# Kernel tuning notes

Measured on AMD Instinct MI355X. Metric: run time of the kernel, lower is better.

## Reference

```python
import jax, jax.numpy as jnp
import numpy as np
from jax import lax

B = 128
NC = 100


def _conv(x, w, b, stride=1, pad=0, groups=1):
    y = lax.conv_general_dilated(x, w, (stride, stride), [(pad, pad), (pad, pad)],
                                 dimension_numbers=('NCHW', 'OIHW', 'NCHW'),
                                 feature_group_count=groups)
    return y + b[None, :, None, None]


def _maxpool(x):
    # kernel 3, stride 2 (ceil_mode is a no-op for 55/27/13 inputs)
    return lax.reduce_window(x, -jnp.inf, lax.max, (1, 1, 3, 3), (1, 1, 2, 2), 'VALID')


def _lrn(x, n=5, alpha=1e-4, beta=0.75, k=1.0):
    # torch.nn.LocalResponseNorm: x / (k + alpha/n * sum_window(x^2))**beta
    s = lax.reduce_window(x * x, 0.0, lax.add, (1, n, 1, 1), (1, 1, 1, 1),
                          [(0, 0), (n // 2, n // 2), (0, 0), (0, 0)])
    return x / (k + (alpha / n) * s) ** beta


def _features(x, w1, b1, w2, b2, w3, b3, w4, b4, w5, b5):
    x = _lrn(_maxpool(jnp.maximum(_conv(x, w1, b1, 4, 0), 0)))
    x = _lrn(_maxpool(jnp.maximum(_conv(x, w2, b2, 1, 2, 2), 0)))
    x = jnp.maximum(_conv(x, w3, b3, 1, 1), 0)
    x = jnp.maximum(_conv(x, w4, b4, 1, 1, 2), 0)
    x = _maxpool(jnp.maximum(_conv(x, w5, b5, 1, 1, 2), 0))
    return x  # [B,256,6,6]


def _head(f, w6, b6, w7, b7, wc, bc):
    h = jnp.maximum(f @ w6.T + b6, 0)
    h = jnp.maximum(h @ w7.T + b7, 0)
    return h @ wc.T + bc


def setup_inputs():
    key = jax.random.key(0)
    ks = jax.random.split(key, 12)
    p = lambda k, s, sc: jax.random.normal(k, s, jnp.float32) * sc
    return {
        'x': jax.random.normal(ks[0], (B, 3, 227, 227), jnp.float32),
        'gt': jax.random.randint(ks[1], (B,), 0, NC),
        'u': jax.random.uniform(ks[2], (B, 36), jnp.float32),
        'flag': 1,
        'w1': p(ks[3], (96, 3, 11, 11), 0.02), 'b1': jnp.zeros((96,), jnp.float32),
        'w2': p(ks[4], (256, 48, 5, 5), 0.02), 'b2': jnp.zeros((256,), jnp.float32),
        'w3': p(ks[5], (384, 256, 3, 3), 0.02), 'b3': jnp.zeros((384,), jnp.float32),
        'w4': p(ks[6], (384, 192, 3, 3), 0.02), 'b4': jnp.zeros((384,), jnp.float32),
        'w5': p(ks[7], (256, 192, 3, 3), 0.02), 'b5': jnp.zeros((256,), jnp.float32),
        'w6': p(ks[8], (4096, 9216), 0.01), 'b6': jnp.zeros((4096,), jnp.float32),
        'w7': p(ks[9], (4096, 4096), 0.01), 'b7': jnp.zeros((4096,), jnp.float32),
        'wc': p(ks[10], (NC, 4096), 0.01), 'bc': jnp.zeros((NC,), jnp.float32),
    }


def reference(x, gt, u, flag, w1, b1, w2, b2, w3, b3, w4, b4, w5, b5,
              w6, b6, w7, b7, wc, bc):
    feat = _features(x * 57.6, w1, b1, w2, b2, w3, b3, w4, b4, w5, b5)
    Bn, C, H, W = feat.shape
    HW = H * W
    head = lambda f: _head(f.reshape(Bn, -1), w6, b6, w7, b7, wc, bc)
    if flag:
        rows = jnp.arange(Bn)
        xn = lax.stop_gradient(feat)  # detached clone in torch
        def score(f):
            out = head(f)
            return jnp.sum(out[rows, gt]), out
        grads, out = jax.grad(score, has_aux=True)(xn)
        # ---- spatial RSC branch (deterministic stand-in for random.randint<=4) ----
        spatial_mean = grads.mean(axis=1).reshape(Bn, HW)
        drop_num = HW // 3  # int(HW/3)
        th = -jnp.sort(-spatial_mean, axis=1)[:, drop_num:drop_num + 1]
        cand = spatial_mean >= th               # high-gradient cells (mask_all==0 in torch)
        sc = jnp.where(cand, u, -1.0)           # npr.choice(zero_index, drop_num) equivalent
        _, idx = lax.top_k(sc, drop_num)
        mask = jnp.ones((Bn, HW), feat.dtype).at[rows[:, None], idx].set(0.0)
        mask_all = mask.reshape(Bn, 1, H, W)
        # ---- keep masks only where dropping them hurts the gt probability ----
        cls_before = jax.nn.softmax(out, axis=1)[rows, gt]
        cls_after = jax.nn.softmax(head(xn * mask_all), axis=1)[rows, gt]
        cv = jnp.maximum(cls_before - cls_after - 1e-4, 0.0)
        th_fg = -jnp.sort(-cv)[int(round(Bn / 3.0))]
        keep_full = ~(cv > th_fg)
        mask_all = jnp.where(keep_full[:, None, None, None], jnp.float32(1.0), mask_all)
        feat = feat * lax.stop_gradient(mask_all)
    return head(feat)
```

## Files before the change

kernel.cpp:

```cpp
#include <hip/hip_runtime.h>

#define CDIV(a,b) (((a)+(b)-1)/(b))

typedef __attribute__((ext_vector_type(8))) short bf16x8;
typedef __attribute__((ext_vector_type(4))) float f32x4;

__device__ __forceinline__ unsigned packsplit(float x) {
    union { float f; unsigned u; } a; a.f = x;
    unsigned r = a.u + 0x7fffu + ((a.u >> 16) & 1u);
    unsigned hi = r & 0xffff0000u;
    union { float f; unsigned u; } b; b.u = hi;
    float res = x - b.f;
    union { float f; unsigned u; } c; c.f = res;
    unsigned r2 = c.u + 0x7fffu + ((c.u >> 16) & 1u);
    return hi | (r2 >> 16);
}
__device__ __forceinline__ unsigned hipair(unsigned a, unsigned b){ return (a>>16)|(b&0xffff0000u); }
__device__ __forceinline__ unsigned lopair(unsigned a, unsigned b){ return (a&0xffffu)|(b<<16); }

__global__ void pack_scale_kernel(const float* __restrict__ src, unsigned* __restrict__ dst,
                                  int n4, float scale)
{
    int i = blockIdx.x * blockDim.x + threadIdx.x;
    if (i >= n4) return;
    float4 v = ((const float4*)src)[i];
    uint4 o;
    o.x = packsplit(v.x * scale); o.y = packsplit(v.y * scale);
    o.z = packsplit(v.z * scale); o.w = packsplit(v.w * scale);
    ((uint4*)dst)[i] = o;
}

__global__ void wsplit_frag(const float* __restrict__ w, short* __restrict__ dst,
                            int G, int cog, int R, int CB, int niter)
{
    int idx = blockIdx.x * blockDim.x + threadIdx.x;
    int total = G * CB * niter * 512;
    if (idx >= total) return;
    int ln = idx & 63;
    int t  = (idx >> 6) & 7;
    int s  = idx >> 9;
    int kt = s % niter;
    int s2 = s / niter;
    int cb = s2 % CB;
    int g  = s2 / CB;
    int row = cb * 128 + t * 16 + (ln & 15);
    int qq = ln >> 4;
    bool rok = row < cog;
    const float* wr = w + (size_t)(g * cog + (rok ? row : 0)) * R;
    short hv[8], lv[8];
    #pragma unroll
    for (int e = 0; e < 8; ++e) {
        int k = kt * 32 + ((e < 4) ? (qq * 4 + e) : (16 + qq * 4 + e - 4));
        float x = (rok && k < R) ? wr[k] : 0.f;
        unsigned p = packsplit(x);
        hv[e] = (short)(p >> 16);
        lv[e] = (short)(p & 0xffffu);
    }
    short* sb = dst + (size_t)s * 8192 + t * 512 + ln * 8;
    *(short4*)(sb)     = make_short4(hv[0], hv[1], hv[2], hv[3]);
    *(short4*)(sb + 4) = make_short4(hv[4], hv[5], hv[6], hv[7]);
    short* sl = sb + 4096;
    *(short4*)(sl)     = make_short4(lv[0], lv[1], lv[2], lv[3]);
    *(short4*)(sl + 4) = make_short4(lv[4], lv[5], lv[6], lv[7]);
}

template<int KSZ, int STRIDE, int PAD, int OUTPACK>
__global__ __launch_bounds__(256, 2) void conv_mfma128(
    const unsigned* __restrict__ in, const short* __restrict__ wtr,
    const float* __restrict__ bs, void* __restrict__ outv,
    int N, int Cin, int Hin, int Win, int Cout, int groups,
    int Hout, int Wout, int CB, int niter)
{
    const int cig = Cin / groups, cog = Cout / groups;
    const int R = cig * KSZ * KSZ;
    const int HW = Hout * Wout;
    const int NSP = N * HW;
    const int g = blockIdx.z;
    const int cb = blockIdx.y;
    const int sp0 = blockIdx.x * 128;
    const int co0 = cb * 128;
    const int tid = threadIdx.x;
    const int lane = tid & 63;
    const int wid = tid >> 6;
    const int wr = wid >> 1, wc = wid & 1;

    __shared__ __align__(16) short Ah[4096];
    __shared__ __align__(16) short Al[4096];
    __shared__ __align__(16) short Bh[4096];
    __shared__ __align__(16) short Bl[4096];

    f32x4 acc[4][4];
    #pragma unroll
    for (int i = 0; i < 4; ++i)
        #pragma unroll
        for (int j = 0; j < 4; ++j)
            acc[i][j] = (f32x4){0.f, 0.f, 0.f, 0.f};

    const int s_ = tid & 127;
    const int qpair = tid >> 7;
    const int spx = sp0 + s_;
    const bool xok = spx < NSP;
    int xn = 0, xho = 0, xwo = 0;
    if (xok) { xn = spx / HW; int pp = spx - xn * HW; xho = pp / Wout; xwo = pp - xho * Wout; }
    const unsigned* inb = in + ((size_t)xn * Cin + (size_t)g * cig) * Hin * Win;
    const int hi0 = xho * STRIDE - PAD, wi0 = xwo * STRIDE - PAD;
    const int bnt = s_ >> 4, bnl = s_ & 15;
    const int lnE = bnl + 32 * qpair;
    const int lnO = lnE + 16;

    const short* slab0 = wtr + (size_t)((g * CB + cb) * niter) * 8192;

    for (int it = 0; it < niter; ++it) {
        const int r0 = it * 32;
        {
            const uint4* src = (const uint4*)(slab0 + (size_t)it * 8192);
            uint4 a0 = src[tid], a1 = src[tid + 256];
            uint4 c0 = src[tid + 512], c1 = src[tid + 768];
            ((uint4*)Ah)[tid] = a0; ((uint4*)Ah)[tid + 256] = a1;
            ((uint4*)Al)[tid] = c0; ((uint4*)Al)[tid + 256] = c1;
        }
        {
            const int kA = r0 + qpair * 8;
            int ciA, khA, kwA, ciB, khB, kwB;
            { int kk = kA;      ciA = kk / (KSZ*KSZ); int rem = kk - ciA*(KSZ*KSZ); khA = rem / KSZ; kwA = rem - khA*KSZ; }
            { int kk = kA + 16; ciB = kk / (KSZ*KSZ); int rem = kk - ciB*(KSZ*KSZ); khB = rem / KSZ; kwB = rem - khB*KSZ; }
            unsigned uA[8], uB[8];
            #pragma unroll
            for (int e = 0; e < 8; ++e) {
                {
                    int hh = hi0 + khA, ww = wi0 + kwA;
                    unsigned v = 0u;
                    if (xok && (kA + e) < R && (unsigned)hh < (unsigned)Hin && (unsigned)ww < (unsigned)Win)
                        v = inb[(size_t)(ciA * Hin + hh) * Win + ww];
                    uA[e] = v;
                    if (++kwA == KSZ) { kwA = 0; if (++khA == KSZ) { khA = 0; ++ciA; } }
                }
                {
                    int hh = hi0 + khB, ww = wi0 + kwB;
                    unsigned v = 0u;
                    if (xok && (kA + 16 + e) < R && (unsigned)hh < (unsigned)Hin && (unsigned)ww < (unsigned)Win)
                        v = inb[(size_t)(ciB * Hin + hh) * Win + ww];
                    uB[e] = v;
                    if (++kwB == KSZ) { kwB = 0; if (++khB == KSZ) { khB = 0; ++ciB; } }
                }
            }
            uint4 d;
            d.x = hipair(uA[0], uA[1]); d.y = hipair(uA[2], uA[3]);
            d.z = hipair(uB[0], uB[1]); d.w = hipair(uB[2], uB[3]);
            ((uint4*)Bh)[bnt * 64 + lnE] = d;
            d.x = hipair(uA[4], uA[5]); d.y = hipair(uA[6], uA[7]);
            d.z = hipair(uB[4], uB[5]); d.w = hipair(uB[6], uB[7]);
            ((uint4*)Bh)[bnt * 64 + lnO] = d;
            d.x = lopair(uA[0], uA[1]); d.y = lopair(uA[2], uA[3]);
            d.z = lopair(uB[0], uB[1]); d.w = lopair(uB[2], uB[3]);
            ((uint4*)Bl)[bnt * 64 + lnE] = d;
            d.x = lopair(uA[4], uA[5]); d.y = lopair(uA[6], uA[7]);
            d.z = lopair(uB[4], uB[5]); d.w = lopair(uB[6], uB[7]);
            ((uint4*)Bl)[bnt * 64 + lnO] = d;
        }
        __syncthreads();
        {
            bf16x8 fah[4], fal[4], fbh[4], fbl[4];
            #pragma unroll
            for (int mi = 0; mi < 4; ++mi) {
                int off = (wr * 4 + mi) * 512 + lane * 8;
                fah[mi] = *(const bf16x8*)(Ah + off);
                fal[mi] = *(const bf16x8*)(Al + off);
            }
            #pragma unroll
            for (int ni = 0; ni < 4; ++ni) {
                int off = (wc * 4 + ni) * 512 + lane * 8;
                fbh[ni] = *(const bf16x8*)(Bh + off);
                fbl[ni] = *(const bf16x8*)(Bl + off);
            }
            #pragma unroll
            for (int mi = 0; mi < 4; ++mi)
                #pragma unroll
                for (int ni = 0; ni < 4; ++ni) {
                    acc[mi][ni] = __builtin_amdgcn_mfma_f32_16x16x32_bf16(fah[mi], fbh[ni], acc[mi][ni], 0, 0, 0);
                    acc[mi][ni] = __builtin_amdgcn_mfma_f32_16x16x32_bf16(fah[mi], fbl[ni], acc[mi][ni], 0, 0, 0);
                    acc[mi][ni] = __builtin_amdgcn_mfma_f32_16x16x32_bf16(fal[mi], fbh[ni], acc[mi][ni], 0, 0, 0);
                }
        }
        __syncthreads();
    }

    const int colc = lane & 15;
    const int rowb = (lane >> 4) * 4;
    #pragma unroll
    for (int ni = 0; ni < 4; ++ni) {
        int sp = sp0 + (wc * 4 + ni) * 16 + colc;
        if (sp >= NSP) continue;
        int n = sp / HW; int pp = sp - n * HW;
        #pragma unroll
        for (int mi = 0; mi < 4; ++mi) {
            #pragma unroll
            for (int j = 0; j < 4; ++j) {
                int cop = co0 + (wr * 4 + mi) * 16 + rowb + j;
                if (cop >= cog) continue;
                int co = g * cog + cop;
                float v = fmaxf(bs[co] + acc[mi][ni][j], 0.f);
                size_t oi = ((size_t)n * Cout + co) * HW + pp;
                if (OUTPACK) ((unsigned*)outv)[oi] = packsplit(v);
                else         ((float*)outv)[oi] = v;
            }
        }
    }
}

__global__ __launch_bounds__(256) void gemm64_nt_k(
    const float* __restrict__ A, const float* __restrict__ W,
    float* __restrict__ part, int M, int N, int K, int kchunk)
{
    const int tx = threadIdx.x, ty = threadIdx.y;
    const int tid = ty * 16 + tx;
    const int m0 = blockIdx.y * 64, n0 = blockIdx.x * 64;
    const int kz = blockIdx.z;
    const int kbeg = kz * kchunk;
    const int kend = min(K, kbeg + kchunk);
    __shared__ float As[16][68], Bs[16][68];
    float acc[4][4] = {};

    const int lr = tid >> 2;
    const int lk4 = (tid & 3) * 4;
    const bool arow_ok = (m0 + lr) < M;
    const bool wrow_ok = (n0 + lr) < N;
    const float* arow = A + (size_t)(m0 + lr) * K;
    const float* wrow = W + (size_t)(n0 + lr) * K;

    for (int k0 = kbeg; k0 < kend; k0 += 16) {
        if (arow_ok && (k0 + lk4 + 3) < kend) {
            float4 v = *(const float4*)(arow + k0 + lk4);
            As[lk4 + 0][lr] = v.x; As[lk4 + 1][lr] = v.y; As[lk4 + 2][lr] = v.z; As[lk4 + 3][lr] = v.w;
        } else {
            #pragma unroll
            for (int q = 0; q < 4; ++q) {
                int k = k0 + lk4 + q;
                As[lk4 + q][lr] = (arow_ok && k < kend) ? arow[k] : 0.f;
            }
        }
        if (wrow_ok && (k0 + lk4 + 3) < kend) {
            float4 v = *(const float4*)(wrow + k0 + lk4);
            Bs[lk4 + 0][lr] = v.x; Bs[lk4 + 1][lr] = v.y; Bs[lk4 + 2][lr] = v.z; Bs[lk4 + 3][lr] = v.w;
        } else {
            #pragma unroll
            for (int q = 0; q < 4; ++q) {
                int k = k0 + lk4 + q;
                Bs[lk4 + q][lr] = (wrow_ok && k < kend) ? wrow[k] : 0.f;
            }
        }
        __syncthreads();
        #pragma unroll
        for (int kk = 0; kk < 16; ++kk) {
            float a[4], b[4];
            *(float4*)a = *(const float4*)&As[kk][ty * 4];
            *(float4*)b = *(const float4*)&Bs[kk][tx * 4];
            #pragma unroll
            for (int i = 0; i < 4; ++i)
                #pragma unroll
                for (int j = 0; j < 4; ++j)
                    acc[i][j] = fmaf(a[i], b[j], acc[i][j]);
        }
        __syncthreads();
    }
    float* pout = part + (size_t)kz * M * N;
    #pragma unroll
    for (int i = 0; i < 4; ++i) {
        int row = m0 + ty * 4 + i;
        if (row >= M) continue;
        #pragma unroll
        for (int j = 0; j < 4; ++j) {
            int col = n0 + tx * 4 + j;
            if (col >= N) continue;
            pout[(size_t)row * N + col] = acc[i][j];
        }
    }
}

__global__ __launch_bounds__(256) void gemm64_nn_k(
    const float* __restrict__ A, const float* __restrict__ W,
    float* __restrict__ part, int M, int N, int K, int kchunk)
{
    const int tx = threadIdx.x, ty = threadIdx.y;
    const int tid = ty * 16 + tx;
    const int m0 = blockIdx.y * 64, n0 = blockIdx.x * 64;
    const int kz = blockIdx.z;
    const int kbeg = kz * kchunk;
    const int kend = min(K, kbeg + kchunk);
    __shared__ float As[16][68], Bs[16][68];
    float acc[4][4] = {};

    const int lr = tid >> 2;
    const int lk4 = (tid & 3) * 4;
    const bool arow_ok = (m0 + lr) < M;
    const float* arow = A + (size_t)(m0 + lr) * K;
    const int bkk = tid >> 4;
    const int bn4 = (tid & 15) * 4;

    for (int k0 = kbeg; k0 < kend; k0 += 16) {
        if (arow_ok && (k0 + lk4 + 3) < kend) {
            float4 v = *(const float4*)(arow + k0 + lk4);
            As[lk4 + 0][lr] = v.x; As[lk4 + 1][lr] = v.y; As[lk4 + 2][lr] = v.z; As[lk4 + 3][lr] = v.w;
        } else {
            #pragma unroll
            for (int q = 0; q < 4; ++q) {
                int k = k0 + lk4 + q;
                As[lk4 + q][lr] = (arow_ok && k < kend) ? arow[k] : 0.f;
            }
        }
        if ((k0 + bkk) < kend && (n0 + bn4 + 3) < N) {
            float4 v = *(const float4*)(W + (size_t)(k0 + bkk) * N + n0 + bn4);
            Bs[bkk][bn4 + 0] = v.x; Bs[bkk][bn4 + 1] = v.y; Bs[bkk][bn4 + 2] = v.z; Bs[bkk][bn4 + 3] = v.w;
        } else {
            #pragma unroll
            for (int q = 0; q < 4; ++q) {
                int col = n0 + bn4 + q;
                Bs[bkk][bn4 + q] = ((k0 + bkk) < kend && col < N) ? W[(size_t)(k0 + bkk) * N + col] : 0.f;
            }
        }
        __syncthreads();
        #pragma unroll
        for (int kk = 0; kk < 16; ++kk) {
            float a[4], b[4];
            *(float4*)a = *(const float4*)&As[kk][ty * 4];
            *(float4*)b = *(const float4*)&Bs[kk][tx * 4];
            #pragma unroll
            for (int i = 0; i < 4; ++i)
                #pragma unroll
                for (int j = 0; j < 4; ++j)
                    acc[i][j] = fmaf(a[i], b[j], acc[i][j]);
        }
        __syncthreads();
    }
    float* pout = part + (size_t)kz * M * N;
    #pragma unroll
    for (int i = 0; i < 4; ++i) {
        int row = m0 + ty * 4 + i;
        if (row >= M) continue;
        #pragma unroll
        for (int j = 0; j < 4; ++j) {
            int col = n0 + tx * 4 + j;
            if (col >= N) continue;
            pout[(size_t)row * N + col] = acc[i][j];
        }
    }
}

__global__ void reduce_parts(const float* __restrict__ part, const float* __restrict__ bias,
                             float* __restrict__ out, int MN, int N, int P, int relu)
{
    int idx = blockIdx.x * blockDim.x + threadIdx.x;
    if (idx >= MN) return;
    float s = 0.f;
    for (int p = 0; p < P; ++p) s += part[(size_t)p * MN + idx];
    if (bias) s += bias[idx % N];
    out[idx] = relu ? fmaxf(s, 0.f) : s;
}

__global__ void maxpool3s2_kernel(const float* __restrict__ in, float* __restrict__ out,
                                  int N, int C, int Hin, int Win, int Hout, int Wout)
{
    int idx = blockIdx.x * blockDim.x + threadIdx.x;
    int total = N * C * Hout * Wout;
    if (idx >= total) return;
    int wo = idx % Wout; int t = idx / Wout;
    int ho = t % Hout; t /= Hout;
    int c = t % C; int n = t / C;
    const float* ip = in + ((size_t)n * C + c) * Hin * Win;
    int h0 = ho * 2, w0 = wo * 2;
    float m = -1e30f;
    for (int dh = 0; dh < 3; ++dh)
        for (int dw = 0; dw < 3; ++dw)
            m = fmaxf(m, ip[(h0 + dh) * Win + (w0 + dw)]);
    out[idx] = m;
}

__global__ void lrn_pack_kernel(float* __restrict__ x, int N, int C, int HW)
{
    int idx = blockIdx.x * blockDim.x + threadIdx.x;
    int total = N * HW;
    if (idx >= total) return;
    int p = idx % HW; int n = idx / HW;
    float* base = x + (size_t)n * C * HW + p;
    unsigned* ubase = (unsigned*)base;
    const float an = 1e-4f / 5.f;
    float r0 = 0.f, r1 = 0.f, r2, r3, r4;
    r2 = base[0];
    r3 = (C > 1) ? base[(size_t)HW] : 0.f;
    r4 = (C > 2) ? base[(size_t)2 * HW] : 0.f;
    float s = r2 * r2 + r3 * r3 + r4 * r4;
    for (int c = 0; c < C; ++c) {
        float y = r2 / powf(1.f + an * s, 0.75f);
        ubase[(size_t)c * HW] = packsplit(y);
        s -= r0 * r0;
        r0 = r1; r1 = r2; r2 = r3; r3 = r4;
        r4 = (c + 3 < C) ? base[(size_t)(c + 3) * HW] : 0.f;
        s += r4 * r4;
    }
}

__global__ void g2m_kernel(const float* __restrict__ wc, const int* __restrict__ gt,
                           const float* __restrict__ h2, float* __restrict__ g2m,
                           int B, int D)
{
    int idx = blockIdx.x * blockDim.x + threadIdx.x;
    if (idx >= B * D) return;
    int b = idx / D, i = idx % D;
    g2m[idx] = (h2[idx] > 0.f) ? wc[(size_t)gt[b] * D + i] : 0.f;
}

__global__ void relumask_kernel(float* __restrict__ g, const float* __restrict__ h, int n)
{
    int idx = blockIdx.x * blockDim.x + threadIdx.x;
    if (idx >= n) return;
    if (h[idx] <= 0.f) g[idx] = 0.f;
}

__global__ void spatial_mean_kernel(const float* __restrict__ gf, float* __restrict__ sm,
                                    int B, int C, int HW)
{
    int idx = blockIdx.x * blockDim.x + threadIdx.x;
    if (idx >= B * HW) return;
    int b = idx / HW, p = idx % HW;
    const float* g = gf + (size_t)b * C * HW + p;
    float s = 0.f;
    for (int c = 0; c < C; ++c) s += g[(size_t)c * HW];
    sm[idx] = s / (float)C;
}

__global__ void rsc_mask_kernel(const float* __restrict__ sm, const float* __restrict__ u,
                                float* __restrict__ mask, int B, int HW, int drop)
{
    int b = blockIdx.x * blockDim.x + threadIdx.x;
    if (b >= B) return;
    const float* s = sm + (size_t)b * HW;
    const float* uu = u + (size_t)b * HW;
    float th = 0.f;
    for (int p = 0; p < HW; ++p) {
        float v = s[p];
        int cg = 0, ce = 0;
        for (int q = 0; q < HW; ++q) { cg += (s[q] > v); ce += (s[q] == v); }
        if (cg <= drop && drop < cg + ce) { th = v; break; }
    }
    float sc[36];
    bool chosen[36];
    for (int p = 0; p < HW; ++p) { sc[p] = (s[p] >= th) ? uu[p] : -1.0f; chosen[p] = false; }
    for (int r = 0; r < drop; ++r) {
        int best = 0; float bv = -1e30f;
        for (int p = 0; p < HW; ++p)
            if (!chosen[p] && sc[p] > bv) { bv = sc[p]; best = p; }
        chosen[best] = true;
    }
    float* m = mask + (size_t)b * HW;
    for (int p = 0; p < HW; ++p) m[p] = chosen[p] ? 0.f : 1.f;
}

__global__ void maskfeat_kernel(const float* __restrict__ feat, const float* __restrict__ mask,
                                float* __restrict__ featb, int B, int CHW, int HW)
{
    int idx = blockIdx.x * blockDim.x + threadIdx.x;
    if (idx >= B * CHW) return;
    int b = idx / CHW, j = idx % CHW;
    featb[idx] = feat[idx] * mask[(size_t)b * HW + (j % HW)];
}

__global__ void cv_kernel(const float* __restrict__ out0, const float* __restrict__ out1,
                          const int* __restrict__ gt, float* __restrict__ cv, int B, int NCc)
{
    int b = blockIdx.x * blockDim.x + threadIdx.x;
    if (b >= B) return;
    const float* a = out0 + (size_t)b * NCc;
    const float* c = out1 + (size_t)b * NCc;
    int g = gt[b];
    float m0 = -1e30f, m1 = -1e30f;
    for (int i = 0; i < NCc; ++i) { m0 = fmaxf(m0, a[i]); m1 = fmaxf(m1, c[i]); }
    float s0 = 0.f, s1 = 0.f;
    for (int i = 0; i < NCc; ++i) { s0 += expf(a[i] - m0); s1 += expf(c[i] - m1); }
    float pb = expf(a[g] - m0) / s0;
    float pa = expf(c[g] - m1) / s1;
    cv[b] = fmaxf(pb - pa - 1e-4f, 0.f);
}

__global__ void final_select_kernel(const float* __restrict__ cv, const float* __restrict__ out0,
                                    const float* __restrict__ out1, const int* __restrict__ flag,
                                    float* __restrict__ out, int B, int NCc, int kidx)
{
    __shared__ float thfg;
    int b = threadIdx.x;
    float v = cv[b];
    int cg = 0, ce = 0;
    for (int j = 0; j < B; ++j) { float w = cv[j]; cg += (w > v); ce += (w == v); }
    if (cg <= kidx && kidx < cg + ce) thfg = v;
    __syncthreads();
    bool keep = !(v > thfg);
    if (*flag == 0) keep = true;
    const float* src = keep ? out0 : out1;
    for (int c = 0; c < NCc; ++c)
        out[(size_t)b * NCc + c] = src[(size_t)b * NCc + c];
}

extern "C" void kernel_launch(void* const* d_in, const int* in_sizes, int n_in,
                              void* d_out, int out_size, void* d_ws, size_t ws_size,
                              hipStream_t stream) {
    const float* x   = (const float*)d_in[0];
    const int*   gt  = (const int*)d_in[1];
    const float* u   = (const float*)d_in[2];
    const int*   flag= (const int*)d_in[3];
    const float* w1  = (const float*)d_in[4];  const float* b1 = (const float*)d_in[5];
    const float* w2  = (const float*)d_in[6];  const float* b2 = (const float*)d_in[7];
    const float* w3  = (const float*)d_in[8];  const float* b3 = (const float*)d_in[9];
    const float* w4  = (const float*)d_in[10]; const float* b4 = (const float*)d_in[11];
    const float* w5  = (const float*)d_in[12]; const float* b5 = (const float*)d_in[13];
    const float* w6  = (const float*)d_in[14]; const float* b6 = (const float*)d_in[15];
    const float* w7  = (const float*)d_in[16]; const float* b7 = (const float*)d_in[17];
    const float* wc  = (const float*)d_in[18]; const float* bc = (const float*)d_in[19];
    float* out = (float*)d_out;
    (void)ws_size; (void)in_sizes; (void)n_in; (void)out_size;

    float* w = (float*)d_ws;
    float* p1   = w;
    float* p2   = p1 + (size_t)8957952;
    float* wtrF = p2 + (size_t)5537792;
    float* Br   = wtrF + (size_t)2572288;
    short* wtrS = (short*)wtrF;

    float*    cbuf1 = Br;
    unsigned* xs    = (unsigned*)(Br + (size_t)9292800);
    float* cbuf2 = Br;
    unsigned* c3s  = (unsigned*)Br;
    unsigned* c4s  = (unsigned*)(Br + (size_t)8306688);
    float* c5out   = Br;
    float* part    = Br + (size_t)8306688;
    float* feat    = Br + (size_t)16613376;
    float* featb   = feat + (size_t)1179648;
    float* h1      = featb + (size_t)1179648;
    float* h2      = h1 + (size_t)524288;
    float* h1b     = h2 + (size_t)524288;
    float* h2b     = h1b + (size_t)524288;
    float* g1      = h2b + (size_t)524288;
    float* g2m     = g1 + (size_t)524288;
    float* gf      = g2m + (size_t)524288;
    float* out0    = gf + (size_t)1179648;
    float* out1    = out0 + 12800;
    float* sm      = out1 + 12800;
    float* mask    = sm + 4608;
    float* cv      = mask + 4608;

    const size_t o1 = 0;
    const size_t o2 = 98304;
    const size_t o3 = 720896;
    const size_t o4 = 2490368;
    const size_t o5 = 4259840;

    wsplit_frag<<<CDIV(1*1*12*512, 256), 256, 0, stream>>>(w1, wtrS + o1, 1,  96,  363, 1, 12);
    wsplit_frag<<<CDIV(2*1*38*512, 256), 256, 0, stream>>>(w2, wtrS + o2, 2, 128, 1200, 1, 38);
    wsplit_frag<<<CDIV(1*3*72*512, 256), 256, 0, stream>>>(w3, wtrS + o3, 1, 384, 2304, 3, 72);
    wsplit_frag<<<CDIV(2*2*54*512, 256), 256, 0, stream>>>(w4, wtrS + o4, 2, 192, 1728, 2, 54);
    wsplit_frag<<<CDIV(2*1*54*512, 256), 256, 0, stream>>>(w5, wtrS + o5, 2, 128, 1728, 1, 54);

    for (int cs = 0; cs < 128; cs += 32) {
        pack_scale_kernel<<<CDIV(1236696, 256), 256, 0, stream>>>(
            x + (size_t)cs * 154587, xs, 1236696, 57.6f);
        conv_mfma128<11, 4, 0, 0><<<dim3(757, 1, 1), 256, 0, stream>>>(
            xs, wtrS + o1, b1, cbuf1, 32, 3, 227, 227, 96, 1, 55, 55, 1, 12);
        maxpool3s2_kernel<<<CDIV(32 * 96 * 729, 256), 256, 0, stream>>>(
            cbuf1, p1 + (size_t)cs * 96 * 729, 32, 96, 55, 55, 27, 27);
    }
    lrn_pack_kernel<<<CDIV(128 * 729, 256), 256, 0, stream>>>(p1, 128, 96, 729);

    conv_mfma128<5, 1, 2, 0><<<dim3(729, 1, 2), 256, 0, stream>>>(
        (const unsigned*)p1, wtrS + o2, b2, cbuf2, 128, 96, 27, 27, 256, 2, 27, 27, 1, 38);
    maxpool3s2_kernel<<<CDIV(128 * 256 * 169, 256), 256, 0, stream>>>(
        cbuf2, p2, 128, 256, 27, 27, 13, 13);
    lrn_pack_kernel<<<CDIV(128 * 169, 256), 256, 0, stream>>>(p2, 128, 256, 169);

    conv_mfma128<3, 1, 1, 1><<<dim3(169, 3, 1), 256, 0, stream>>>(
        (const unsigned*)p2, wtrS + o3, b3, c3s, 128, 256, 13, 13, 384, 1, 13, 13, 3, 72);
    conv_mfma128<3, 1, 1, 1><<<dim3(169, 2, 2), 256, 0, stream>>>(
        c3s, wtrS + o4, b4, c4s, 128, 384, 13, 13, 384, 2, 13, 13, 2, 54);
    conv_mfma128<3, 1, 1, 0><<<dim3(169, 1, 2), 256, 0, stream>>>(
        c4s, wtrS + o5, b5, c5out, 128, 384, 13, 13, 256, 2, 13, 13, 1, 54);
    maxpool3s2_kernel<<<CDIV(128 * 256 * 36, 256), 256, 0, stream>>>(
        c5out, feat, 128, 256, 13, 13, 6, 6);

    dim3 blk(16, 16);
    gemm64_nt_k<<<dim3(64, 2, 8), blk, 0, stream>>>(feat, w6, part, 128, 4096, 9216, 1152);
    reduce_parts<<<CDIV(128 * 4096, 256), 256, 0, stream>>>(part, b6, h1, 128 * 4096, 4096, 8, 1);
    gemm64_nt_k<<<dim3(64, 2, 8), blk, 0, stream>>>(h1, w7, part, 128, 4096, 4096, 512);
    reduce_parts<<<CDIV(128 * 4096, 256), 256, 0, stream>>>(part, b7, h2, 128 * 4096, 4096, 8, 1);
    gemm64_nt_k<<<dim3(2, 2, 8), blk, 0, stream>>>(h2, wc, part, 128, 100, 4096, 512);
    reduce_parts<<<CDIV(128 * 100, 256), 256, 0, stream>>>(part, bc, out0, 128 * 100, 100, 8, 0);

    g2m_kernel<<<CDIV(128 * 4096, 256), 256, 0, stream>>>(wc, gt, h2, g2m, 128, 4096);
    gemm64_nn_k<<<dim3(64, 2, 8), blk, 0, stream>>>(g2m, w7, part, 128, 4096, 4096, 512);
    reduce_parts<<<CDIV(128 * 4096, 256), 256, 0, stream>>>(part, nullptr, g1, 128 * 4096, 4096, 8, 0);
    relumask_kernel<<<CDIV(128 * 4096, 256), 256, 0, stream>>>(g1, h1, 128 * 4096);
    gemm64_nn_k<<<dim3(144, 2, 4), blk, 0, stream>>>(g1, w6, part, 128, 9216, 4096, 1024);
    reduce_parts<<<CDIV(128 * 9216, 256), 256, 0, stream>>>(part, nullptr, gf, 128 * 9216, 9216, 4, 0);

    spatial_mean_kernel<<<CDIV(128 * 36, 128), 128, 0, stream>>>(gf, sm, 128, 256, 36);
    rsc_mask_kernel<<<2, 64, 0, stream>>>(sm, u, mask, 128, 36, 12);

    maskfeat_kernel<<<CDIV(128 * 9216, 256), 256, 0, stream>>>(feat, mask, featb, 128, 9216, 36);
    gemm64_nt_k<<<dim3(64, 2, 8), blk, 0, stream>>>(featb, w6, part, 128, 4096, 9216, 1152);
    reduce_parts<<<CDIV(128 * 4096, 256), 256, 0, stream>>>(part, b6, h1b, 128 * 4096, 4096, 8, 1);
    gemm64_nt_k<<<dim3(64, 2, 8), blk, 0, stream>>>(h1b, w7, part, 128, 4096, 4096, 512);
    reduce_parts<<<CDIV(128 * 4096, 256), 256, 0, stream>>>(part, b7, h2b, 128 * 4096, 4096, 8, 1);
    gemm64_nt_k<<<dim3(2, 2, 8), blk, 0, stream>>>(h2b, wc, part, 128, 100, 4096, 512);
    reduce_parts<<<CDIV(128 * 100, 256), 256, 0, stream>>>(part, bc, out1, 128 * 100, 100, 8, 0);

    cv_kernel<<<1, 128, 0, stream>>>(out0, out1, gt, cv, 128, 100);
    final_select_kernel<<<1, 128, 0, stream>>>(cv, out0, out1, flag, out, 128, 100, 43);
}
```

Measured before the change: 2.792 ms.

## Move FC head GEMMs to split-bf16 MFMA and parallelize RSC mask selection

```diff
diff --git a/kernel.cpp b/kernel.cpp
--- a/kernel.cpp
+++ b/kernel.cpp
@@ -208,6 +208,115 @@
     }
 }
 
+template<int WNN>
+__global__ __launch_bounds__(256, 2) void gemm_mfma_k(
+    const unsigned* __restrict__ act, const float* __restrict__ W,
+    float* __restrict__ part, int N, int K, int kchunk)
+{
+    const int n0 = blockIdx.y * 128;
+    const int kz = blockIdx.z;
+    const int kbeg = kz * kchunk;
+    const int kend = kbeg + kchunk;
+    const int tid = threadIdx.x;
+    const int lane = tid & 63;
+    const int wid = tid >> 6;
+    const int wr = wid >> 1, wc2 = wid & 1;
+
+    __shared__ __align__(16) short Ah[4096];
+    __shared__ __align__(16) short Al[4096];
+    __shared__ __align__(16) short Bh[4096];
+    __shared__ __align__(16) short Bl[4096];
+
+    f32x4 acc[4][4];
+    #pragma unroll
+    for (int i = 0; i < 4; ++i)
+        #pragma unroll
+        for (int j = 0; j < 4; ++j)
+            acc[i][j] = (f32x4){0.f, 0.f, 0.f, 0.f};
+
+    const int rr = tid >> 1;
+    const int kq = (tid & 1) * 16;
+    const int dsoff = (rr >> 4) * 512 + (rr & 15) * 8 + (kq ? 4 : 0);
+    short* dAh = Ah + dsoff; short* dAl = Al + dsoff;
+    short* dBh = Bh + dsoff; short* dBl = Bl + dsoff;
+    const unsigned* actrow = act + (size_t)rr * K + kq;
+
+    for (int k0 = kbeg; k0 < kend; k0 += 32) {
+        {
+            float wv[16];
+            if (!WNN) {
+                const float* src = W + (size_t)(n0 + rr) * K + k0 + kq;
+                #pragma unroll
+                for (int q4 = 0; q4 < 4; ++q4) {
+                    float4 v = *(const float4*)(src + q4 * 4);
+                    wv[q4*4+0] = v.x; wv[q4*4+1] = v.y; wv[q4*4+2] = v.z; wv[q4*4+3] = v.w;
+                }
+            } else {
+                const float* src = W + (size_t)(k0 + kq) * N + n0 + rr;
+                #pragma unroll
+                for (int j = 0; j < 16; ++j) wv[j] = src[(size_t)j * N];
+            }
+            #pragma unroll
+            for (int q4 = 0; q4 < 4; ++q4) {
+                unsigned p0 = packsplit(wv[q4*4+0]), p1 = packsplit(wv[q4*4+1]);
+                unsigned p2 = packsplit(wv[q4*4+2]), p3 = packsplit(wv[q4*4+3]);
+                *(short4*)(dAh + q4*128) = make_short4((short)(p0>>16),(short)(p1>>16),(short)(p2>>16),(short)(p3>>16));
+                *(short4*)(dAl + q4*128) = make_short4((short)(p0&0xffff),(short)(p1&0xffff),(short)(p2&0xffff),(short)(p3&0xffff));
+            }
+        }
+        {
+            const uint4* s = (const uint4*)(actrow + k0);
+            #pragma unroll
+            for (int q4 = 0; q4 < 4; ++q4) {
+                uint4 u = s[q4];
+                *(short4*)(dBh + q4*128) = make_short4((short)(u.x>>16),(short)(u.y>>16),(short)(u.z>>16),(short)(u.w>>16));
+                *(short4*)(dBl + q4*128) = make_short4((short)(u.x&0xffff),(short)(u.y&0xffff),(short)(u.z&0xffff),(short)(u.w&0xffff));
+            }
+        }
+        __syncthreads();
+        {
+            bf16x8 fah[4], fal[4], fbh[4], fbl[4];
+            #pragma unroll
+            for (int mi = 0; mi < 4; ++mi) {
+                int off = (wr * 4 + mi) * 512 + lane * 8;
+                fah[mi] = *(const bf16x8*)(Ah + off);
+                fal[mi] = *(const bf16x8*)(Al + off);
+            }
+            #pragma unroll
+            for (int ni = 0; ni < 4; ++ni) {
+                int off = (wc2 * 4 + ni) * 512 + lane * 8;
+                fbh[ni] = *(const bf16x8*)(Bh + off);
+                fbl[ni] = *(const bf16x8*)(Bl + off);
+            }
+            #pragma unroll
+            for (int mi = 0; mi < 4; ++mi)
+                #pragma unroll
+                for (int ni = 0; ni < 4; ++ni) {
+                    acc[mi][ni] = __builtin_amdgcn_mfma_f32_16x16x32_bf16(fah[mi], fbh[ni], acc[mi][ni], 0, 0, 0);
+                    acc[mi][ni] = __builtin_amdgcn_mfma_f32_16x16x32_bf16(fah[mi], fbl[ni], acc[mi][ni], 0, 0, 0);
+                    acc[mi][ni] = __builtin_amdgcn_mfma_f32_16x16x32_bf16(fal[mi], fbh[ni], acc[mi][ni], 0, 0, 0);
+                }
+        }
+        __syncthreads();
+    }
+
+    const int colc = lane & 15;
+    const int rowb = (lane >> 4) * 4;
+    float* pout = part + (size_t)kz * 128 * N;
+    #pragma unroll
+    for (int ni = 0; ni < 4; ++ni) {
+        int m = (wc2 * 4 + ni) * 16 + colc;
+        #pragma unroll
+        for (int mi = 0; mi < 4; ++mi) {
+            #pragma unroll
+            for (int j = 0; j < 4; ++j) {
+                int n = n0 + (wr * 4 + mi) * 16 + rowb + j;
+                pout[(size_t)m * N + n] = acc[mi][ni][j];
+            }
+        }
+    }
+}
+
 __global__ __launch_bounds__(256) void gemm64_nt_k(
     const float* __restrict__ A, const float* __restrict__ W,
     float* __restrict__ part, int M, int N, int K, int kchunk)
@@ -277,84 +386,18 @@
     }
 }
 
-__global__ __launch_bounds__(256) void gemm64_nn_k(
-    const float* __restrict__ A, const float* __restrict__ W,
-    float* __restrict__ part, int M, int N, int K, int kchunk)
-{
-    const int tx = threadIdx.x, ty = threadIdx.y;
-    const int tid = ty * 16 + tx;
-    const int m0 = blockIdx.y * 64, n0 = blockIdx.x * 64;
-    const int kz = blockIdx.z;
-    const int kbeg = kz * kchunk;
-    const int kend = min(K, kbeg + kchunk);
-    __shared__ float As[16][68], Bs[16][68];
-    float acc[4][4] = {};
-
-    const int lr = tid >> 2;
-    const int lk4 = (tid & 3) * 4;
-    const bool arow_ok = (m0 + lr) < M;
-    const float* arow = A + (size_t)(m0 + lr) * K;
-    const int bkk = tid >> 4;
-    const int bn4 = (tid & 15) * 4;
-
-    for (int k0 = kbeg; k0 < kend; k0 += 16) {
-        if (arow_ok && (k0 + lk4 + 3) < kend) {
-            float4 v = *(const float4*)(arow + k0 + lk4);
-            As[lk4 + 0][lr] = v.x; As[lk4 + 1][lr] = v.y; As[lk4 + 2][lr] = v.z; As[lk4 + 3][lr] = v.w;
-        } else {
-            #pragma unroll
-            for (int q = 0; q < 4; ++q) {
-                int k = k0 + lk4 + q;
-                As[lk4 + q][lr] = (arow_ok && k < kend) ? arow[k] : 0.f;
-            }
-        }
-        if ((k0 + bkk) < kend && (n0 + bn4 + 3) < N) {
-            float4 v = *(const float4*)(W + (size_t)(k0 + bkk) * N + n0 + bn4);
-            Bs[bkk][bn4 + 0] = v.x; Bs[bkk][bn4 + 1] = v.y; Bs[bkk][bn4 + 2] = v.z; Bs[bkk][bn4 + 3] = v.w;
-        } else {
-            #pragma unroll
-            for (int q = 0; q < 4; ++q) {
-                int col = n0 + bn4 + q;
-                Bs[bkk][bn4 + q] = ((k0 + bkk) < kend && col < N) ? W[(size_t)(k0 + bkk) * N + col] : 0.f;
-            }
-        }
-        __syncthreads();
-        #pragma unroll
-        for (int kk = 0; kk < 16; ++kk) {
-            float a[4], b[4];
-            *(float4*)a = *(const float4*)&As[kk][ty * 4];
-            *(float4*)b = *(const float4*)&Bs[kk][tx * 4];
-            #pragma unroll
-            for (int i = 0; i < 4; ++i)
-                #pragma unroll
-                for (int j = 0; j < 4; ++j)
-                    acc[i][j] = fmaf(a[i], b[j], acc[i][j]);
-        }
-        __syncthreads();
-    }
-    float* pout = part + (size_t)kz * M * N;
-    #pragma unroll
-    for (int i = 0; i < 4; ++i) {
-        int row = m0 + ty * 4 + i;
-        if (row >= M) continue;
-        #pragma unroll
-        for (int j = 0; j < 4; ++j) {
-            int col = n0 + tx * 4 + j;
-            if (col >= N) continue;
-            pout[(size_t)row * N + col] = acc[i][j];
-        }
-    }
-}
-
 __global__ void reduce_parts(const float* __restrict__ part, const float* __restrict__ bias,
-                             float* __restrict__ out, int MN, int N, int P, int relu)
+                             float* __restrict__ outf, unsigned* __restrict__ pk,
+                             int MN, int N, int P, int relu)
 {
     int idx = blockIdx.x * blockDim.x + threadIdx.x;
     if (idx >= MN) return;
     float s = 0.f;
     for (int p = 0; p < P; ++p) s += part[(size_t)p * MN + idx];
     if (bias) s += bias[idx % N];
-    out[idx] = relu ? fmaxf(s, 0.f) : s;
+    if (relu) s = fmaxf(s, 0.f);
+    if (outf) outf[idx] = s;
+    if (pk) pk[idx] = packsplit(s);
 }
 
 __global__ void maxpool3s2_kernel(const float* __restrict__ in, float* __restrict__ out,
@@ -399,21 +442,22 @@
     }
 }
 
-__global__ void g2m_kernel(const float* __restrict__ wc, const int* __restrict__ gt,
-                           const float* __restrict__ h2, float* __restrict__ g2m,
-                           int B, int D)
+__global__ void g2m_pack_kernel(const float* __restrict__ wc, const int* __restrict__ gt,
+                                const float* __restrict__ h2, unsigned* __restrict__ g2mp,
+                                int B, int D)
 {
     int idx = blockIdx.x * blockDim.x + threadIdx.x;
     if (idx >= B * D) return;
     int b = idx / D, i = idx % D;
-    g2m[idx] = (h2[idx] > 0.f) ? wc[(size_t)gt[b] * D + i] : 0.f;
-}
-
-__global__ void relumask_kernel(float* __restrict__ g, const float* __restrict__ h, int n)
+    g2mp[idx] = packsplit((h2[idx] > 0.f) ? wc[(size_t)gt[b] * D + i] : 0.f);
+}
+
+__global__ void relupack_kernel(const float* __restrict__ g, const float* __restrict__ h,
+                                unsigned* __restrict__ gp, int n)
 {
     int idx = blockIdx.x * blockDim.x + threadIdx.x;
     if (idx >= n) return;
-    if (h[idx] <= 0.f) g[idx] = 0.f;
+    gp[idx] = packsplit((h[idx] > 0.f) ? g[idx] : 0.f);
 }
 
 __global__ void spatial_mean_kernel(const float* __restrict__ gf, float* __restrict__ sm,
@@ -429,39 +473,39 @@
 }
 
 __global__ void rsc_mask_kernel(const float* __restrict__ sm, const float* __restrict__ u,
-                                float* __restrict__ mask, int B, int HW, int drop)
-{
-    int b = blockIdx.x * blockDim.x + threadIdx.x;
-    if (b >= B) return;
-    const float* s = sm + (size_t)b * HW;
-    const float* uu = u + (size_t)b * HW;
-    float th = 0.f;
-    for (int p = 0; p < HW; ++p) {
+                                float* __restrict__ mask, int HW, int drop)
+{
+    int b = blockIdx.x;
+    int p = threadIdx.x;
+    __shared__ float s[64], uu[64];
+    __shared__ float th;
+    if (p < HW) { s[p] = sm[(size_t)b * HW + p]; uu[p] = u[(size_t)b * HW + p]; }
+    __syncthreads();
+    if (p < HW) {
         float v = s[p];
         int cg = 0, ce = 0;
         for (int q = 0; q < HW; ++q) { cg += (s[q] > v); ce += (s[q] == v); }
-        if (cg <= drop && drop < cg + ce) { th = v; break; }
-    }
-    float sc[36];
-    bool chosen[36];
-    for (int p = 0; p < HW; ++p) { sc[p] = (s[p] >= th) ? uu[p] : -1.0f; chosen[p] = false; }
-    for (int r = 0; r < drop; ++r) {
-        int best = 0; float bv = -1e30f;
-        for (int p = 0; p < HW; ++p)
-            if (!chosen[p] && sc[p] > bv) { bv = sc[p]; best = p; }
-        chosen[best] = true;
-    }
-    float* m = mask + (size_t)b * HW;
-    for (int p = 0; p < HW; ++p) m[p] = chosen[p] ? 0.f : 1.f;
-}
-
-__global__ void maskfeat_kernel(const float* __restrict__ feat, const float* __restrict__ mask,
-                                float* __restrict__ featb, int B, int CHW, int HW)
+        if (cg <= drop && drop < cg + ce) th = v;
+    }
+    __syncthreads();
+    if (p < HW) {
+        float v = (s[p] >= th) ? uu[p] : -1.0f;
+        int rank = 0;
+        for (int q = 0; q < HW; ++q) {
+            float w = (s[q] >= th) ? uu[q] : -1.0f;
+            rank += (w > v) || (w == v && q < p);
+        }
+        mask[(size_t)b * HW + p] = (rank < drop) ? 0.f : 1.f;
+    }
+}
+
+__global__ void maskfeat_pack_kernel(const float* __restrict__ feat, const float* __restrict__ mask,
+                                     unsigned* __restrict__ featbp, int B, int CHW, int HW)
 {
     int idx = blockIdx.x * blockDim.x + threadIdx.x;
     if (idx >= B * CHW) return;
     int b = idx / CHW, j = idx % CHW;
-    featb[idx] = feat[idx] * mask[(size_t)b * HW + (j % HW)];
+    featbp[idx] = packsplit(feat[idx] * mask[(size_t)b * HW + (j % HW)]);
 }
 
 __global__ void cv_kernel(const float* __restrict__ out0, const float* __restrict__ out1,
@@ -531,20 +575,20 @@
     unsigned* c4s  = (unsigned*)(Br + (size_t)8306688);
     float* c5out   = Br;
     float* part    = Br + (size_t)8306688;
-    float* feat    = Br + (size_t)16613376;
-    float* featb   = feat + (size_t)1179648;
-    float* h1      = featb + (size_t)1179648;
-    float* h2      = h1 + (size_t)524288;
-    float* h1b     = h2 + (size_t)524288;
-    float* h2b     = h1b + (size_t)524288;
-    float* g1      = h2b + (size_t)524288;
-    float* g2m     = g1 + (size_t)524288;
-    float* gf      = g2m + (size_t)524288;
-    float* out0    = gf + (size_t)1179648;
-    float* out1    = out0 + 12800;
-    float* sm      = out1 + 12800;
-    float* mask    = sm + 4608;
-    float* cv      = mask + 4608;
+    float*    feat  = Br + (size_t)16613376;
+    unsigned* fp_sh = (unsigned*)(feat + 1179648);
+    float*    h1    = (float*)(fp_sh + 1179648);
+    unsigned* h1p   = (unsigned*)(h1 + 524288);
+    float*    h2    = (float*)(h1p + 524288);
+    float*    sA    = h2 + 524288;
+    unsigned* sB    = (unsigned*)(sA + 524288);
+    unsigned* g1p   = sB + 524288;
+    float*    gf    = (float*)(g1p + 524288);
+    float*    out0  = gf + 1179648;
+    float*    out1  = out0 + 12800;
+    float*    sm    = out1 + 12800;
+    float*    mask  = sm + 4608;
+    float*    cv    = mask + 4608;
 
     const size_t o1 = 0;
     const size_t o2 = 98304;
@@ -583,31 +627,31 @@
     maxpool3s2_kernel<<<CDIV(128 * 256 * 36, 256), 256, 0, stream>>>(
         c5out, feat, 128, 256, 13, 13, 6, 6);
 
-    dim3 blk(16, 16);
-    gemm64_nt_k<<<dim3(64, 2, 8), blk, 0, stream>>>(feat, w6, part, 128, 4096, 9216, 1152);
-    reduce_parts<<<CDIV(128 * 4096, 256), 256, 0, stream>>>(part, b6, h1, 128 * 4096, 4096, 8, 1);
-    gemm64_nt_k<<<dim3(64, 2, 8), blk, 0, stream>>>(h1, w7, part, 128, 4096, 4096, 512);
-    reduce_parts<<<CDIV(128 * 4096, 256), 256, 0, stream>>>(part, b7, h2, 128 * 4096, 4096, 8, 1);
-    gemm64_nt_k<<<dim3(2, 2, 8), blk, 0, stream>>>(h2, wc, part, 128, 100, 4096, 512);
-    reduce_parts<<<CDIV(128 * 100, 256), 256, 0, stream>>>(part, bc, out0, 128 * 100, 100, 8, 0);
-
-    g2m_kernel<<<CDIV(128 * 4096, 256), 256, 0, stream>>>(wc, gt, h2, g2m, 128, 4096);
-    gemm64_nn_k<<<dim3(64, 2, 8), blk, 0, stream>>>(g2m, w7, part, 128, 4096, 4096, 512);
-    reduce_parts<<<CDIV(128 * 4096, 256), 256, 0, stream>>>(part, nullptr, g1, 128 * 4096, 4096, 8, 0);
-    relumask_kernel<<<CDIV(128 * 4096, 256), 256, 0, stream>>>(g1, h1, 128 * 4096);
-    gemm64_nn_k<<<dim3(144, 2, 4), blk, 0, stream>>>(g1, w6, part, 128, 9216, 4096, 1024);
-    reduce_parts<<<CDIV(128 * 9216, 256), 256, 0, stream>>>(part, nullptr, gf, 128 * 9216, 9216, 4, 0);
+    pack_scale_kernel<<<CDIV(294912, 256), 256, 0, stream>>>(feat, fp_sh, 294912, 1.f);
+    gemm_mfma_k<0><<<dim3(1, 32, 8), 256, 0, stream>>>(fp_sh, w6, part, 4096, 9216, 1152);
+    reduce_parts<<<CDIV(128 * 4096, 256), 256, 0, stream>>>(part, b6, h1, h1p, 128 * 4096, 4096, 8, 1);
+    gemm_mfma_k<0><<<dim3(1, 32, 8), 256, 0, stream>>>(h1p, w7, part, 4096, 4096, 512);
+    reduce_parts<<<CDIV(128 * 4096, 256), 256, 0, stream>>>(part, b7, h2, nullptr, 128 * 4096, 4096, 8, 1);
+    gemm64_nt_k<<<dim3(2, 2, 8), dim3(16, 16), 0, stream>>>(h2, wc, part, 128, 100, 4096, 512);
+    reduce_parts<<<CDIV(128 * 100, 256), 256, 0, stream>>>(part, bc, out0, nullptr, 128 * 100, 100, 8, 0);
+
+    g2m_pack_kernel<<<CDIV(128 * 4096, 256), 256, 0, stream>>>(wc, gt, h2, sB, 128, 4096);
+    gemm_mfma_k<1><<<dim3(1, 32, 8), 256, 0, stream>>>(sB, w7, part, 4096, 4096, 512);
+    reduce_parts<<<CDIV(128 * 4096, 256), 256, 0, stream>>>(part, nullptr, sA, nullptr, 128 * 4096, 4096, 8, 0);
+    relupack_kernel<<<CDIV(128 * 4096, 256), 256, 0, stream>>>(sA, h1, g1p, 128 * 4096);
+    gemm_mfma_k<1><<<dim3(1, 72, 4), 256, 0, stream>>>(g1p, w6, part, 9216, 4096, 1024);
+    reduce_parts<<<CDIV(128 * 9216, 256), 256, 0, stream>>>(part, nullptr, gf, nullptr, 128 * 9216, 9216, 4, 0);
 
     spatial_mean_kernel<<<CDIV(128 * 36, 128), 128, 0, stream>>>(gf, sm, 128, 256, 36);
-    rsc_mask_kernel<<<2, 64, 0, stream>>>(sm, u, mask, 128, 36, 12);
-
-    maskfeat_kernel<<<CDIV(128 * 9216, 256), 256, 0, stream>>>(feat, mask, featb, 128, 9216, 36);
-    gemm64_nt_k<<<dim3(64, 2, 8), blk, 0, stream>>>(featb, w6, part, 128, 4096, 9216, 1152);
-    reduce_parts<<<CDIV(128 * 4096, 256), 256, 0, stream>>>(part, b6, h1b, 128 * 4096, 4096, 8, 1);
-    gemm64_nt_k<<<dim3(64, 2, 8), blk, 0, stream>>>(h1b, w7, part, 128, 4096, 4096, 512);
-    reduce_parts<<<CDIV(128 * 4096, 256), 256, 0, stream>>>(part, b7, h2b, 128 * 4096, 4096, 8, 1);
-    gemm64_nt_k<<<dim3(2, 2, 8), blk, 0, stream>>>(h2b, wc, part, 128, 100, 4096, 512);
-    reduce_parts<<<CDIV(128 * 100, 256), 256, 0, stream>>>(part, bc, out1, 128 * 100, 100, 8, 0);
+    rsc_mask_kernel<<<128, 64, 0, stream>>>(sm, u, mask, 36, 12);
+
+    maskfeat_pack_kernel<<<CDIV(128 * 9216, 256), 256, 0, stream>>>(feat, mask, fp_sh, 128, 9216, 36);
+    gemm_mfma_k<0><<<dim3(1, 32, 8), 256, 0, stream>>>(fp_sh, w6, part, 4096, 9216, 1152);
+    reduce_parts<<<CDIV(128 * 4096, 256), 256, 0, stream>>>(part, b6, nullptr, sB, 128 * 4096, 4096, 8, 1);
+    gemm_mfma_k<0><<<dim3(1, 32, 8), 256, 0, stream>>>(sB, w7, part, 4096, 4096, 512);
+    reduce_parts<<<CDIV(128 * 4096, 256), 256, 0, stream>>>(part, b7, sA, nullptr, 128 * 4096, 4096, 8, 1);
+    gemm64_nt_k<<<dim3(2, 2, 8), dim3(16, 16), 0, stream>>>(sA, wc, part, 128, 100, 4096, 512);
+    reduce_parts<<<CDIV(128 * 100, 256), 256, 0, stream>>>(part, bc, out1, nullptr, 128 * 100, 100, 8, 0);
 
     cv_kernel<<<1, 128, 0, stream>>>(out0, out1, gt, cv, 128, 100);
     final_select_kernel<<<1, 128, 0, stream>>>(cv, out0, out1, flag, out, 128, 100, 43);
```

Result: faster. 2.273 ms (-18.6%).
